# Performance work log

Measured on AMD Instinct MI355X. Metric: run time of the kernel, lower is better.

## Reference

```python
import jax, jax.numpy as jnp
import numpy as np

BASE = 10000.0

def _rope(x):
    # x: [b, n, h, d]; positions along token axis n, rotate-half convention
    d = x.shape[-1]
    n = x.shape[1]
    inv_freq = 1.0 / (BASE ** (jnp.arange(0, d, 2, dtype=jnp.float32) / d))  # [d/2]
    t = jnp.arange(n, dtype=jnp.float32)
    freqs = jnp.outer(t, inv_freq)                       # [n, d/2]
    emb = jnp.concatenate([freqs, freqs], axis=-1)       # [n, d]
    cos = jnp.cos(emb)[None, :, None, :]
    sin = jnp.sin(emb)[None, :, None, :]
    x1, x2 = jnp.split(x, 2, axis=-1)
    rot = jnp.concatenate([-x2, x1], axis=-1)
    return x * cos + rot * sin


def setup_inputs() -> dict:
    key = jax.random.key(0)
    k1, k2, k3 = jax.random.split(key, 3)
    b, c, hh, ww = 64, 1024, 16, 16
    x = jax.random.normal(k1, (b, c, hh, ww), dtype=jnp.float32)
    w_qkv = jax.random.normal(k2, (3 * c, c), dtype=jnp.float32) * 0.02
    w_lin = jax.random.normal(k3, (c, c, 1, 1), dtype=jnp.float32) * 0.02
    b_lin = jnp.zeros((c,), dtype=jnp.float32)
    return {"x": x, "w_qkv": w_qkv, "w_lin": w_lin, "b_lin": b_lin, "n_heads": 16}


def reference(x, w_qkv, w_lin, b_lin, n_heads):
    b, c, hh, ww = x.shape
    n = hh * ww
    d_head = c // n_heads
    scale = d_head ** -0.5
    # flatten(2).transpose(-2,-1): [b, n, c]
    xt = jnp.transpose(x.reshape(b, c, n), (0, 2, 1))
    # qkv proj, unflatten to [b, n, heads, 3*d_head], chunk along last dim
    qkv = (xt @ w_qkv.T).reshape(b, n, n_heads, 3 * d_head)
    q, k, v = jnp.split(qkv, 3, axis=-1)                  # each [b, n, h, d]
    q = _rope(q)
    k = _rope(k)
    q = jax.nn.softmax(q, axis=-1) * scale                # softmax over d_head
    k = jax.nn.softmax(k, axis=-2)                        # softmax over heads axis (as in torch code)
    # k^T @ v over the heads axis -> per-token [d_head, d_head] context
    context = jnp.einsum('bnhd,bnhe->bnde', k, v)
    o = jnp.einsum('bnhd,bnde->bnhe', q, context)         # [b, n, h, d]
    # transpose(-2,-1).reshape(b, c, h, w)
    o = jnp.transpose(o, (0, 1, 3, 2)).reshape(b, c, hh, ww)
    # 1x1 conv
    return jnp.einsum('bchw,oc->bohw', o, w_lin[:, :, 0, 0]) + b_lin[None, :, None, None]
```

## Files before the change

### kernel.cpp

```cpp
#include <hip/hip_runtime.h>
#include <hip/hip_bf16.h>
#include <math.h>

typedef __hip_bfloat16 hbf16;
typedef __attribute__((ext_vector_type(8))) __bf16    bf16x8;
typedef __attribute__((ext_vector_type(4))) float     f32x4;
typedef __attribute__((ext_vector_type(4))) _Float16  f16x4;
typedef __attribute__((ext_vector_type(8))) unsigned short u16x8;

#define C_    1024
#define NTOK  256
#define NH    16
#define J3    3072

__device__ __forceinline__ unsigned short fbits(float v){
    return __builtin_bit_cast(unsigned short, __float2bfloat16(v));
}
__device__ __forceinline__ __bf16 to_bf(float v){
    return __builtin_bit_cast(__bf16, __float2bfloat16(v));
}

__device__ __forceinline__ void gload_lds16(const __bf16* g, __bf16* l) {
    __builtin_amdgcn_global_load_lds((const __attribute__((address_space(1))) void*)g,
                                     (__attribute__((address_space(3))) void*)l, 16, 0, 0);
}

__global__ __launch_bounds__(256) void cvt_w(const float* __restrict__ wq,
                                             __bf16* __restrict__ wqo,
                                             const float* __restrict__ wl,
                                             __bf16* __restrict__ wlo) {
    const float* in; __bf16* out; int i;
    if (blockIdx.x < 3072) { in = wq; out = wqo; i = blockIdx.x * 256 + threadIdx.x; }
    else                   { in = wl; out = wlo; i = (blockIdx.x - 3072) * 256 + threadIdx.x; }
    float4 v = ((const float4*)in)[i];
    ushort4 u;
    u.x = fbits(v.x); u.y = fbits(v.y); u.z = fbits(v.z); u.w = fbits(v.w);
    ((ushort4*)out)[i] = u;
}

__global__ __launch_bounds__(256) void xpose_x(const float* __restrict__ X,
                                               __bf16* __restrict__ Xt) {
    __shared__ float t[32][36];
    const int b = blockIdx.z, k0 = blockIdx.y * 32, s0 = blockIdx.x * 32;
    const int tid = threadIdx.x;
    {
        int kl = tid >> 3, s4 = (tid & 7) * 4;
        float4 v = *(const float4*)(X + ((size_t)b << 18) + (size_t)(k0 + kl) * 256 + s0 + s4);
        t[kl][s4] = v.x; t[kl][s4 + 1] = v.y; t[kl][s4 + 2] = v.z; t[kl][s4 + 3] = v.w;
    }
    __syncthreads();
    {
        int sl = tid >> 3, k4 = (tid & 7) * 4;
        ushort4 u;
        u.x = fbits(t[k4][sl]); u.y = fbits(t[k4 + 1][sl]);
        u.z = fbits(t[k4 + 2][sl]); u.w = fbits(t[k4 + 3][sl]);
        *(ushort4*)(Xt + (size_t)(b * 256 + s0 + sl) * 1024 + k0 + k4) = u;
    }
}

#define WAITVM_I(N) asm volatile("s_waitcnt vmcnt(" #N ")" ::: "memory")
#define WAITVM(N) WAITVM_I(N)

#define BARRIER()                                                              \
    __builtin_amdgcn_sched_barrier(0);                                         \
    __builtin_amdgcn_s_barrier();                                              \
    __builtin_amdgcn_sched_barrier(0)

__device__ __forceinline__ void stage16(const __bf16* __restrict__ G,
                                        __bf16* l, int kk, int wave, int lane) {
    const int rl = lane >> 2;
    const int cg = (lane & 3) ^ ((lane >> 3) & 3);
    const int row = wave * 16 + rl;
    gload_lds16(G + ((size_t)row << 10) + kk + cg * 8, l + wave * 512);
}

#define STEP(BUF, S, DOSTG, VM)                                                \
  {                                                                            \
    WAITVM(VM);                                                                \
    BARRIER();                                                                 \
    const __bf16* sa_ = sm.kl[BUF] + aoff;                                     \
    const __bf16* sb_ = sm.kl[BUF] + 8192 + boff;                              \
    bf16x8 afr[4], bfr[4];                                                     \
    _Pragma("unroll") for (int i = 0; i < 4; ++i) {                            \
      afr[i] = *(const bf16x8*)(sa_ + i * 512);                                \
      bfr[i] = *(const bf16x8*)(sb_ + i * 512);                                \
    }                                                                          \
    __builtin_amdgcn_s_setprio(1);                                             \
    _Pragma("unroll") for (int mi = 0; mi < 4; ++mi)                           \
      _Pragma("unroll") for (int ni = 0; ni < 4; ++ni)                         \
        acc[mi][ni] = __builtin_amdgcn_mfma_f32_16x16x32_bf16(                 \
            afr[mi], bfr[ni], acc[mi][ni], 0, 0, 0);                           \
    __builtin_amdgcn_s_setprio(0);                                             \
    BARRIER();                                                                 \
    if (DOSTG) {                                                               \
      stage16(Ab, &sm.kl[BUF][0],    ((S) + 2) << 5, wave, lane);              \
      stage16(Bb, &sm.kl[BUF][8192], ((S) + 2) << 5, wave, lane);              \
    }                                                                          \
  }

template <int EPI>
__global__ __launch_bounds__(1024, 4) void gemm256(const __bf16* __restrict__ A,
                                                   const __bf16* __restrict__ B,
                                                   void* __restrict__ Cout,
                                                   const float* __restrict__ bias) {
    __shared__ union __align__(16) {
        __bf16 kl[2][16384];
        __bf16 st[128][264];
    } sm;

    const int tid  = threadIdx.x;
    const int wave = tid >> 6, lane = tid & 63;
    const int wm = wave >> 2, wn = wave & 3;
    const int quad = lane >> 4, m = lane & 15;

    const int wg = blockIdx.x;
    int mb, nb;
    if (EPI == 0) {
        const int local = wg >> 3;
        mb = (wg & 7) * 8 + (local & 7);
        nb = local >> 3;
    } else {
        const int local = wg >> 3;
        mb = local & 3;
        nb = (wg & 7) * 8 + (local >> 2);
    }
    const int m0 = mb << 8, n0 = nb << 8;

    const __bf16* Ab = A + ((size_t)m0 << 10);
    const __bf16* Bb = B + ((size_t)n0 << 10);

    const int pcs  = quad ^ ((m >> 1) & 3);
    const int aoff = (wm * 64 + m) * 32 + pcs * 8;
    const int boff = (wn * 64 + m) * 32 + pcs * 8;

    f32x4 acc[4][4] = {};

    stage16(Ab, &sm.kl[0][0],    0,  wave, lane);
    stage16(Bb, &sm.kl[0][8192], 0,  wave, lane);
    stage16(Ab, &sm.kl[1][0],    32, wave, lane);
    stage16(Bb, &sm.kl[1][8192], 32, wave, lane);

    for (int tt = 0; tt < 28; tt += 2) {
        STEP(0, tt + 0, 1, 2)
        STEP(1, tt + 1, 1, 2)
    }
    STEP(0, 28, 1, 2)
    STEP(1, 29, 1, 2)
    STEP(0, 30, 0, 2)
    STEP(1, 31, 0, 0)

    if (EPI == 0) {
        __syncthreads();
        __bf16* Y = (__bf16*)Cout;
        #pragma unroll
        for (int h = 0; h < 2; ++h) {
            if ((wm >> 1) == h) {
                #pragma unroll
                for (int mi = 0; mi < 4; ++mi)
                    #pragma unroll
                    for (int ni = 0; ni < 4; ++ni) {
                        const int r = (wm & 1) * 64 + mi * 16 + quad * 4;
                        const int c = wn * 64 + ni * 16 + m;
                        #pragma unroll
                        for (int j = 0; j < 4; ++j)
                            sm.st[r + j][c] = to_bf(acc[mi][ni][j]);
                    }
            }
            __syncthreads();
            #pragma unroll
            for (int i = 0; i < 4; ++i) {
                const int cid = i * 1024 + tid;
                const int r = cid >> 5, ch = (cid & 31) * 8;
                *(bf16x8*)(Y + (size_t)(m0 + h * 128 + r) * 3072 + n0 + ch) =
                    *(const bf16x8*)&sm.st[r][ch];
            }
            __syncthreads();
        }
    } else {
        float* outp = (float*)Cout;
        const int rbase = m0 + wm * 64 + quad * 4;
        const int nbase = n0 + wn * 64 + m;
        #pragma unroll
        for (int mi = 0; mi < 4; ++mi) {
            float bia[4];
            #pragma unroll
            for (int j = 0; j < 4; ++j) bia[j] = bias[rbase + mi * 16 + j];
            #pragma unroll
            for (int ni = 0; ni < 4; ++ni) {
                const int nn = nbase + ni * 16;
                const size_t base = ((size_t)(nn >> 8) << 18) + (nn & 255);
                #pragma unroll
                for (int j = 0; j < 4; ++j) {
                    const int oc = rbase + mi * 16 + j;
                    outp[base + ((size_t)oc << 8)] = acc[mi][ni][j] + bia[j];
                }
            }
        }
    }
}

__global__ __launch_bounds__(1024) void attn_mfma(const __bf16* __restrict__ Y,
                                                  __bf16* __restrict__ Ot) {
    __shared__ union __align__(16) {
        __bf16  v[16][1024];
        ushort4 ost[256][16];
    } sm;

    const int tid  = threadIdx.x;
    const int wave = tid >> 6, lane = tid & 63;
    const int bb = blockIdx.x >> 4;
    const int n0 = (blockIdx.x & 15) * 16;
    const int n  = n0 + wave;
    const int quad = lane >> 4, m = lane & 15;
    const __bf16* Yt = Y + (size_t)(bb * 256 + n) * J3;

    #pragma unroll
    for (int p = 0; p < 2; ++p) {
        const int h = p * 8 + (lane >> 3), part = lane & 7;
        gload_lds16(Yt + h * 192 + 128 + part * 8, &sm.v[wave][p * 512]);
    }

    bf16x8 qb[2], kb[2];
    #pragma unroll
    for (int st = 0; st < 2; ++st) {
        qb[st] = *(const bf16x8*)(Yt + m * 192 +      st * 32 + quad * 8);
        kb[st] = *(const bf16x8*)(Yt + m * 192 + 64 + st * 32 + quad * 8);
    }
    float qf[16], kf[16];
    #pragma unroll
    for (int st = 0; st < 2; ++st)
        #pragma unroll
        for (int j = 0; j < 8; ++j) {
            qf[st * 8 + j] = (float)qb[st][j];
            kf[st * 8 + j] = (float)kb[st][j];
        }

    const float fn = (float)n;
    #pragma unroll
    for (int j = 0; j < 8; ++j) {
        const float d  = (float)(quad * 8 + j);
        const float th = fn * __expf(-0.28782313662425572f * d);
        const float sn = __sinf(th), cn = __cosf(th);
        float a0 = qf[j], a1 = qf[8 + j];
        qf[j]     = a0 * cn - a1 * sn;
        qf[8 + j] = a1 * cn + a0 * sn;
        float b0 = kf[j], b1 = kf[8 + j];
        kf[j]     = b0 * cn - b1 * sn;
        kf[8 + j] = b1 * cn + b0 * sn;
    }

    float qe[16], ls = 0.f;
    #pragma unroll
    for (int i = 0; i < 16; ++i) { qe[i] = __expf(qf[i]); ls += qe[i]; }
    ls += __shfl_xor(ls, 16);
    ls += __shfl_xor(ls, 32);
    const float qinv = 0.125f * __builtin_amdgcn_rcpf(ls);
    bf16x8 qbh[2];
    #pragma unroll
    for (int st = 0; st < 2; ++st)
        #pragma unroll
        for (int j = 0; j < 8; ++j) qbh[st][j] = to_bf(qe[st * 8 + j] * qinv);

    float ke[16], kc[16];
    #pragma unroll
    for (int i = 0; i < 16; ++i) { ke[i] = __expf(kf[i]); kc[i] = ke[i]; }
    #pragma unroll
    for (int msk = 1; msk <= 8; msk <<= 1)
        #pragma unroll
        for (int i = 0; i < 16; ++i) kc[i] += __shfl_xor(kc[i], msk);
    bf16x8 kbh[2];
    #pragma unroll
    for (int st = 0; st < 2; ++st)
        #pragma unroll
        for (int j = 0; j < 8; ++j)
            kbh[st][j] = to_bf(ke[st * 8 + j] * __builtin_amdgcn_rcpf(kc[st * 8 + j]));

    f32x4 Sp = {0.f, 0.f, 0.f, 0.f};
    Sp = __builtin_amdgcn_mfma_f32_16x16x32_bf16(kbh[0], qbh[0], Sp, 0, 0, 0);
    Sp = __builtin_amdgcn_mfma_f32_16x16x32_bf16(kbh[1], qbh[1], Sp, 0, 0, 0);

    __syncthreads();

    f32x4 o4[4];
#if __has_builtin(__builtin_amdgcn_mfma_f32_16x16x16f16)
    f16x4 af;
    #pragma unroll
    for (int r = 0; r < 4; ++r) af[r] = (_Float16)Sp[r];
    #pragma unroll
    for (int tile = 0; tile < 4; ++tile) {
        f16x4 bv;
        #pragma unroll
        for (int j = 0; j < 4; ++j)
            bv[j] = (_Float16)(float)sm.v[wave][(quad * 4 + j) * 64 + tile * 16 + m];
        f32x4 z = {0.f, 0.f, 0.f, 0.f};
        o4[tile] = __builtin_amdgcn_mfma_f32_16x16x16f16(af, bv, z, 0, 0, 0);
    }
#else
    bf16x8 a2;
    #pragma unroll
    for (int j = 0; j < 8; ++j) {
        int k = quad * 8 + j;
        int src = ((k & 15) >> 2) * 16 + m;
        float v = __shfl(Sp[k & 3], src, 64);
        a2[j] = (quad < 2) ? to_bf(v) : to_bf(0.f);
    }
    #pragma unroll
    for (int tile = 0; tile < 4; ++tile) {
        bf16x8 bv;
        #pragma unroll
        for (int j = 0; j < 8; ++j) {
            int k = quad * 8 + j;
            int kk = (k < 16) ? k : 0;
            bv[j] = sm.v[wave][kk * 64 + tile * 16 + m];
        }
        f32x4 z = {0.f, 0.f, 0.f, 0.f};
        o4[tile] = __builtin_amdgcn_mfma_f32_16x16x32_bf16(a2, bv, z, 0, 0, 0);
    }
#endif

    __syncthreads();

    #pragma unroll
    for (int r = 0; r < 4; ++r) {
        const int s = m * 16 + quad * 4 + r;
        const int phys = wave ^ (quad * 4 + r) ^ m;
        ushort4 u;
        u.x = fbits(o4[0][r]); u.y = fbits(o4[1][r]);
        u.z = fbits(o4[2][r]); u.w = fbits(o4[3][r]);
        sm.ost[s][phys] = u;
    }
    __syncthreads();

    {
        const int row = tid >> 2;
        const int w0  = (tid & 3) * 4;
        ushort4 u4[4];
        #pragma unroll
        for (int j = 0; j < 4; ++j) {
            const int phys = (w0 + j) ^ (row & 15) ^ (row >> 4);
            u4[j] = sm.ost[row][phys];
        }
        __bf16* dst = Ot + (((size_t)(bb * 256 + row)) << 10) + n0 * 4 + w0 * 4;
        u16x8 a = {u4[0].x, u4[0].y, u4[0].z, u4[0].w, u4[1].x, u4[1].y, u4[1].z, u4[1].w};
        u16x8 b = {u4[2].x, u4[2].y, u4[2].z, u4[2].w, u4[3].x, u4[3].y, u4[3].z, u4[3].w};
        *(u16x8*)dst = a;
        *(u16x8*)(dst + 8) = b;
    }
}

extern "C" void kernel_launch(void* const* d_in, const int* in_sizes, int n_in,
                              void* d_out, int out_size, void* d_ws, size_t ws_size,
                              hipStream_t stream) {
    const float* x     = (const float*)d_in[0];
    const float* w_qkv = (const float*)d_in[1];
    const float* w_lin = (const float*)d_in[2];
    const float* b_lin = (const float*)d_in[3];
    float* out = (float*)d_out;

    char* ws = (char*)d_ws;
    __bf16* Y    = (__bf16*)ws;
    __bf16* XtOt = (__bf16*)(ws + (size_t)100663296);
    __bf16* Wqb  = (__bf16*)(ws + (size_t)134217728);
    __bf16* Wlb  = (__bf16*)(ws + (size_t)140509184);

    cvt_w<<<4096, 256, 0, stream>>>(w_qkv, Wqb, w_lin, Wlb);
    xpose_x<<<dim3(8, 32, 64), 256, 0, stream>>>(x, XtOt);

    gemm256<0><<<768, 1024, 0, stream>>>(XtOt, Wqb, (void*)Y, nullptr);
    attn_mfma<<<1024, 1024, 0, stream>>>(Y, XtOt);
    gemm256<1><<<256, 1024, 0, stream>>>(Wlb, XtOt, (void*)out, b_lin);
}
```

Baseline: 313.2 us.

## Replace direct global-to-LDS loads with register-staged prefetch pipeline in GEMM

The GEMM main loop no longer uses global_load_lds DMA into a double-buffered LDS. It now prefetches tiles into registers two steps ahead, then writes them to LDS after compute, with an lgkmcnt wait and an extra barrier per step. The launch-bounds occupancy hint drops from 4 to 2, which gives more registers for the prefetch buffers. The workgroup-to-tile swizzle is also changed for both GEMM variants. This trades higher register pressure and extra VGPR-to-LDS stores for a deeper global-memory prefetch.

```diff
diff --git a/kernel.cpp b/kernel.cpp
--- a/kernel.cpp
+++ b/kernel.cpp
@@ -58,26 +58,28 @@
     }
 }
 
-#define WAITVM_I(N) asm volatile("s_waitcnt vmcnt(" #N ")" ::: "memory")
-#define WAITVM(N) WAITVM_I(N)
-
 #define BARRIER()                                                              \
     __builtin_amdgcn_sched_barrier(0);                                         \
     __builtin_amdgcn_s_barrier();                                              \
     __builtin_amdgcn_sched_barrier(0)
 
-__device__ __forceinline__ void stage16(const __bf16* __restrict__ G,
-                                        __bf16* l, int kk, int wave, int lane) {
+#define LGKM0() asm volatile("s_waitcnt lgkmcnt(0)" ::: "memory")
+
+__device__ __forceinline__ bf16x8 gld(const __bf16* __restrict__ G,
+                                      int kk, int wave, int lane) {
     const int rl = lane >> 2;
     const int cg = (lane & 3) ^ ((lane >> 3) & 3);
     const int row = wave * 16 + rl;
-    gload_lds16(G + ((size_t)row << 10) + kk + cg * 8, l + wave * 512);
-}
-
-#define STEP(BUF, S, DOSTG, VM)                                                \
+    return *(const bf16x8*)(G + ((size_t)row << 10) + kk + cg * 8);
+}
+__device__ __forceinline__ void stw(__bf16* buf, int wave, int lane,
+                                    bf16x8 va, bf16x8 vb) {
+    *(bf16x8*)(buf + wave * 512 + lane * 8) = va;
+    *(bf16x8*)(buf + 8192 + wave * 512 + lane * 8) = vb;
+}
+
+#define STEP(BUF, S, RA, RB, DOW, DOL)                                         \
   {                                                                            \
-    WAITVM(VM);                                                                \
-    BARRIER();                                                                 \
     const __bf16* sa_ = sm.kl[BUF] + aoff;                                     \
     const __bf16* sb_ = sm.kl[BUF] + 8192 + boff;                              \
     bf16x8 afr[4], bfr[4];                                                     \
@@ -91,15 +93,20 @@
         acc[mi][ni] = __builtin_amdgcn_mfma_f32_16x16x32_bf16(                 \
             afr[mi], bfr[ni], acc[mi][ni], 0, 0, 0);                           \
     __builtin_amdgcn_s_setprio(0);                                             \
-    BARRIER();                                                                 \
-    if (DOSTG) {                                                               \
-      stage16(Ab, &sm.kl[BUF][0],    ((S) + 2) << 5, wave, lane);              \
-      stage16(Bb, &sm.kl[BUF][8192], ((S) + 2) << 5, wave, lane);              \
+    BARRIER();                                   \
+    if (DOW) {                                                                 \
+      stw(sm.kl[BUF], wave, lane, RA, RB);        \
+      if (DOL) {                                                               \
+        RA = gld(Ab, ((S) + 4) << 5, wave, lane);                              \
+        RB = gld(Bb, ((S) + 4) << 5, wave, lane);                              \
+      }                                                                        \
+      LGKM0();                                                                 \
     }                                                                          \
+    BARRIER();                                             \
   }
 
 template <int EPI>
-__global__ __launch_bounds__(1024, 4) void gemm256(const __bf16* __restrict__ A,
+__global__ __launch_bounds__(1024, 2) void gemm256(const __bf16* __restrict__ A,
                                                    const __bf16* __restrict__ B,
                                                    void* __restrict__ Cout,
                                                    const float* __restrict__ bias) {
@@ -116,13 +123,11 @@
     const int wg = blockIdx.x;
     int mb, nb;
     if (EPI == 0) {
-        const int local = wg >> 3;
-        mb = (wg & 7) * 8 + (local & 7);
-        nb = local >> 3;
+        const int gg = (wg & 7) * 96 + (wg >> 3);
+        mb = gg & 63;  nb = gg >> 6;
     } else {
-        const int local = wg >> 3;
-        mb = local & 3;
-        nb = (wg & 7) * 8 + (local >> 2);
+        const int gg = (wg & 7) * 32 + (wg >> 3);
+        mb = gg & 3;   nb = gg >> 2;
     }
     const int m0 = mb << 8, n0 = nb << 8;
 
@@ -135,19 +140,23 @@
 
     f32x4 acc[4][4] = {};
 
-    stage16(Ab, &sm.kl[0][0],    0,  wave, lane);
-    stage16(Bb, &sm.kl[0][8192], 0,  wave, lane);
-    stage16(Ab, &sm.kl[1][0],    32, wave, lane);
-    stage16(Bb, &sm.kl[1][8192], 32, wave, lane);
+    bf16x8 pa = gld(Ab, 0,  wave, lane), pb = gld(Bb, 0,  wave, lane);
+    bf16x8 qa = gld(Ab, 32, wave, lane), qb = gld(Bb, 32, wave, lane);
+    stw(sm.kl[0], wave, lane, pa, pb);
+    pa = gld(Ab, 64, wave, lane); pb = gld(Bb, 64, wave, lane);
+    stw(sm.kl[1], wave, lane, qa, qb);
+    qa = gld(Ab, 96, wave, lane); qb = gld(Bb, 96, wave, lane);
+    LGKM0();
+    BARRIER();
 
     for (int tt = 0; tt < 28; tt += 2) {
-        STEP(0, tt + 0, 1, 2)
-        STEP(1, tt + 1, 1, 2)
-    }
-    STEP(0, 28, 1, 2)
-    STEP(1, 29, 1, 2)
-    STEP(0, 30, 0, 2)
-    STEP(1, 31, 0, 0)
+        STEP(0, tt + 0, pa, pb, 1, 1)
+        STEP(1, tt + 1, qa, qb, 1, 1)
+    }
+    STEP(0, 28, pa, pb, 1, 0)
+    STEP(1, 29, qa, qb, 1, 0)
+    STEP(0, 30, pa, pb, 0, 0)
+    STEP(1, 31, qa, qb, 0, 0)
 
     if (EPI == 0) {
         __syncthreads();
```

After: 312.0 us. No clear change (-0.4%).
